# Optimization experiments

Measured on AMD Instinct MI355X. Metric: run time of the kernel, lower is better.

The kernel has to match this reference:

```python
import jax, jax.numpy as jnp
import numpy as np

N_NODES = 100000
N_EDGES = 1000000
D_IN = 64
D_OUT = 64


def setup_inputs() -> dict:
    key = jax.random.key(0)
    k_x, k_e, k_wl, k_bl, k_wr = jax.random.split(key, 5)
    x = jax.random.normal(k_x, (N_NODES, D_IN), dtype=jnp.float32)
    edge_index = jax.random.randint(k_e, (2, N_EDGES), 0, N_NODES, dtype=jnp.int64)
    scale = 1.0 / np.sqrt(D_IN)
    # SAGEConv params: lin_l (neighbor path, with bias), lin_r (root/self path, no bias)
    W_l = jax.random.uniform(k_wl, (D_OUT, D_IN), dtype=jnp.float32, minval=-scale, maxval=scale)
    b_l = jax.random.uniform(k_bl, (D_OUT,), dtype=jnp.float32, minval=-scale, maxval=scale)
    W_r = jax.random.uniform(k_wr, (D_OUT, D_IN), dtype=jnp.float32, minval=-scale, maxval=scale)
    return {"x": x, "edge_index": edge_index, "W_l": W_l, "b_l": b_l, "W_r": W_r}


def reference(x, edge_index, W_l, b_l, W_r):
    # PyG SAGEConv with mean aggregation:
    #   out = lin_l(mean_{j in N(i)} x_j) + lin_r(x_i);  then ReLU (from GCN.forward)
    src = edge_index[0]  # message sources
    dst = edge_index[1]  # aggregation targets
    n = x.shape[0]
    msg = x[src]  # [E, D_IN] gather
    agg = jax.ops.segment_sum(msg, dst, num_segments=n)  # [N, D_IN]
    deg = jax.ops.segment_sum(jnp.ones((src.shape[0],), x.dtype), dst, num_segments=n)
    mean = agg / jnp.maximum(deg, 1.0)[:, None]  # isolated nodes -> 0
    out = mean @ W_l.T + b_l + x @ W_r.T
    return jax.nn.relu(out)
```

## Files before the change

### kernel.cpp

```cpp
#include <hip/hip_runtime.h>

#define N_NODES 100000
#define N_EDGES 1000000
#define D 64

#define NFINE 782
#define CAP2 1536
#define CHUNK 4096
#define EDGE_BLOCKS 245
#define CONV_BLOCKS 6250
#define CONS_BLOCKS 1564
#define STR 132
#define SCAP 1024

typedef unsigned short u16;
typedef unsigned int u32;
using bf16x8 = __attribute__((ext_vector_type(8))) short;
using f32x4  = __attribute__((ext_vector_type(4))) float;

__device__ __forceinline__ u16 f2bf(float f) {
    u32 u = __float_as_uint(f);
    return (u16)((u + 0x7FFF + ((u >> 16) & 1)) >> 16);
}
__device__ __forceinline__ float bf2f(u16 v) {
    return __uint_as_float(((u32)v) << 16);
}

__global__ __launch_bounds__(256) void conv_zero_kernel(
    const float* __restrict__ x, u16* __restrict__ xb,
    int* __restrict__ cur2) {
    if (blockIdx.x == CONV_BLOCKS) {
        for (int j = threadIdx.x; j < NFINE; j += 256) cur2[j] = 0;
        return;
    }
    int i = blockIdx.x * 256 + threadIdx.x;
    float4 v = ((const float4*)x)[i];
    ((ushort4*)xb)[i] = make_ushort4(f2bf(v.x), f2bf(v.y), f2bf(v.z), f2bf(v.w));
}

__global__ __launch_bounds__(1024) void build3_kernel(
    const int* __restrict__ ei, int* __restrict__ cur2,
    u32* __restrict__ pairs2) {
    __shared__ u32 sorted[CHUNK];
    __shared__ u16 binof[CHUNK];
    __shared__ int hist[NFINE];
    __shared__ int off_l[NFINE];
    __shared__ int cur_l[NFINE];
    __shared__ int base_g[NFINE];
    __shared__ int wsum[16];

    int b = blockIdx.x;
    int t = threadIdx.x;
    int ln = t & 63;
    int wv = t >> 6;

    const u32* uu = (const u32*)ei;
    int f = 1;
    #pragma unroll
    for (int i = 1; i < 16; i += 2)
        if (uu[i] != 0u) f = 0;

    if (t < NFINE) hist[t] = 0;
    __syncthreads();

    int e0 = b * CHUNK;
    int e1 = min(e0 + CHUNK, N_EDGES);
    int ne = e1 - e0;

    const uint2* e64 = (const uint2*)ei;
    int srcv[4], dstv[4];
    #pragma unroll
    for (int i = 0; i < 4; i++) {
        int ee = e0 + t + i * 1024;
        bool ok = ee < e1;
        if (f) {
            uint2 sv = ok ? e64[ee] : make_uint2(0u, 0u);
            uint2 dv = ok ? e64[N_EDGES + ee] : make_uint2(0u, 0u);
            srcv[i] = (int)sv.x;
            dstv[i] = ok ? (int)dv.x : -1;
        } else {
            srcv[i] = ok ? ei[ee] : 0;
            dstv[i] = ok ? ei[N_EDGES + ee] : -1;
        }
    }
    #pragma unroll
    for (int i = 0; i < 4; i++)
        if (dstv[i] >= 0) atomicAdd(&hist[dstv[i] >> 7], 1);
    __syncthreads();

    int h = (t < NFINE) ? hist[t] : 0;
    int inc = h;
    #pragma unroll
    for (int o = 1; o < 64; o <<= 1) {
        int v = __shfl_up(inc, o);
        if (ln >= o) inc += v;
    }
    if (ln == 63) wsum[wv] = inc;
    __syncthreads();
    if (t < 16) {
        int w = wsum[t];
        int winc = w;
        #pragma unroll
        for (int o = 1; o < 16; o <<= 1) {
            int v = __shfl_up(winc, o);
            if (t >= o) winc += v;
        }
        wsum[t] = winc - w;
    }
    __syncthreads();
    if (t < NFINE) {
        int ex = inc - h + wsum[wv];
        off_l[t] = ex;
        cur_l[t] = ex;
        base_g[t] = h ? atomicAdd(&cur2[t], h) : 0;
    }
    __syncthreads();

    #pragma unroll
    for (int i = 0; i < 4; i++) {
        if (dstv[i] >= 0) {
            int fine = dstv[i] >> 7;
            int slot = atomicAdd(&cur_l[fine], 1);
            sorted[slot] = (u32)srcv[i] | ((u32)(dstv[i] & 127) << 17);
            binof[slot] = (u16)fine;
        }
    }
    __syncthreads();

    for (int i = t; i < ne; i += 1024) {
        int fine = binof[i];
        int pos = base_g[fine] + (i - off_l[fine]);
        if (pos < CAP2)
            pairs2[(size_t)fine * CAP2 + pos] = sorted[i];
    }
}

__global__ __launch_bounds__(512, 8) void cons4_kernel(
    const u16* __restrict__ xb, const float* __restrict__ Wl,
    const float* __restrict__ bl, const float* __restrict__ Wr,
    const int* __restrict__ cur2, const u32* __restrict__ pairs2,
    float* __restrict__ out) {
    __shared__ u16 Bs[64 * STR];
    __shared__ u16 As[64 * STR];
    __shared__ int sorted_s[SCAP];
    __shared__ int deg_l[64];
    __shared__ int off_l[64];
    __shared__ int cur_l[64];

    int tid = threadIdx.x;
    int bin = blockIdx.x >> 1;
    int half = blockIdx.x & 1;
    int nbase = bin * 128 + half * 64;
    if (nbase >= N_NODES) return;

    int lane = tid & 63;
    int wv = tid >> 6;

    int cnt = min(cur2[bin], CAP2);
    const u32* pb = &pairs2[(size_t)bin * CAP2];
    u32 ve[3];
    #pragma unroll
    for (int i = 0; i < 3; i++) {
        int e = tid + i * 512;
        ve[i] = (e < cnt) ? pb[e] : 0xFFFFFFFFu;
    }

    if (tid < 64) { deg_l[tid] = 0; cur_l[tid] = 0; }
    if (tid == 0) sorted_s[0] = 0;

    if (tid < 256) {
        int row = tid >> 2;
        int seg = tid & 3;
        const float4* wlf = (const float4*)Wl;
        const float4* wrf = (const float4*)Wr;
        #pragma unroll
        for (int j = 0; j < 4; j++) {
            float4 a = wlf[row * 16 + seg * 4 + j];
            float4 bq = wrf[row * 16 + seg * 4 + j];
            *(ushort4*)&Bs[row * STR + seg * 16 + j * 4] =
                make_ushort4(f2bf(a.x), f2bf(a.y), f2bf(a.z), f2bf(a.w));
            *(ushort4*)&Bs[row * STR + 64 + seg * 16 + j * 4] =
                make_ushort4(f2bf(bq.x), f2bf(bq.y), f2bf(bq.z), f2bf(bq.w));
        }
    }
    __syncthreads();

    #pragma unroll
    for (int i = 0; i < 3; i++) {
        u32 v = ve[i];
        if ((int)(v >> 23) == half) atomicAdd(&deg_l[(v >> 17) & 63], 1);
    }
    __syncthreads();

    if (tid < 64) {
        int dd = deg_l[tid];
        int inc = dd;
        #pragma unroll
        for (int o = 1; o < 64; o <<= 1) {
            int v = __shfl_up(inc, o);
            if (lane >= o) inc += v;
        }
        off_l[tid] = inc - dd;
    }
    __syncthreads();

    #pragma unroll
    for (int i = 0; i < 3; i++) {
        u32 v = ve[i];
        if ((int)(v >> 23) == half) {
            int ln = (v >> 17) & 63;
            int p = off_l[ln] + atomicAdd(&cur_l[ln], 1);
            if (p < SCAP) sorted_s[p] = (int)(v & 0x1FFFFu);
        }
    }
    __syncthreads();

    int nl8 = lane >> 3;
    int c = lane & 7;
    int nl = wv * 8 + nl8;
    int n = nbase + nl;
    int d = deg_l[nl];
    int st = off_l[nl];

    int maxd = d;
    maxd = max(maxd, __shfl_xor(maxd, 8));
    maxd = max(maxd, __shfl_xor(maxd, 16));
    maxd = max(maxd, __shfl_xor(maxd, 32));

    float acc[8];
    #pragma unroll
    for (int j = 0; j < 8; j++) acc[j] = 0.0f;

    int dm1 = (d > 0) ? (d - 1) : 0;
    int sb = (d > 0) ? st : 0;
    for (int k = 0; k < maxd; k += 4) {
        int i0 = sb + min(k + 0, dm1);
        int i1 = sb + min(k + 1, dm1);
        int i2 = sb + min(k + 2, dm1);
        int i3 = sb + min(k + 3, dm1);
        int s0 = sorted_s[i0];
        int s1 = sorted_s[i1];
        int s2 = sorted_s[i2];
        int s3 = sorted_s[i3];
        bf16x8 r0 = *(const bf16x8*)&xb[(size_t)s0 * D + c * 8];
        bf16x8 r1 = *(const bf16x8*)&xb[(size_t)s1 * D + c * 8];
        bf16x8 r2 = *(const bf16x8*)&xb[(size_t)s2 * D + c * 8];
        bf16x8 r3 = *(const bf16x8*)&xb[(size_t)s3 * D + c * 8];
        float m0 = (k + 0 < d) ? 1.0f : 0.0f;
        float m1 = (k + 1 < d) ? 1.0f : 0.0f;
        float m2 = (k + 2 < d) ? 1.0f : 0.0f;
        float m3 = (k + 3 < d) ? 1.0f : 0.0f;
        #pragma unroll
        for (int j = 0; j < 8; j++)
            acc[j] = fmaf(m0, bf2f((u16)r0[j]), acc[j]);
        #pragma unroll
        for (int j = 0; j < 8; j++)
            acc[j] = fmaf(m1, bf2f((u16)r1[j]), acc[j]);
        #pragma unroll
        for (int j = 0; j < 8; j++)
            acc[j] = fmaf(m2, bf2f((u16)r2[j]), acc[j]);
        #pragma unroll
        for (int j = 0; j < 8; j++)
            acc[j] = fmaf(m3, bf2f((u16)r3[j]), acc[j]);
    }

    float inv = (d > 0) ? (1.0f / (float)d) : 0.0f;
    bf16x8 p;
    #pragma unroll
    for (int j = 0; j < 8; j++) p[j] = (short)f2bf(acc[j] * inv);
    *(bf16x8*)&As[nl * STR + c * 8] = p;
    bf16x8 xr = {0, 0, 0, 0, 0, 0, 0, 0};
    if (n < N_NODES) xr = *(const bf16x8*)&xb[(size_t)n * D + c * 8];
    *(bf16x8*)&As[nl * STR + 64 + c * 8] = xr;
    __syncthreads();

    int mtile = wv >> 1;
    int nt0 = (wv & 1) * 2;
    int lrow = lane & 15;
    int quad = lane >> 4;

    const u16* Ab  = &As[(mtile * 16 + lrow) * STR + quad * 8];
    const u16* Bb0 = &Bs[((nt0 + 0) * 16 + lrow) * STR + quad * 8];
    const u16* Bb1 = &Bs[((nt0 + 1) * 16 + lrow) * STR + quad * 8];

    float bias0 = bl[(nt0 + 0) * 16 + lrow];
    float bias1 = bl[(nt0 + 1) * 16 + lrow];
    f32x4 acc0 = {bias0, bias0, bias0, bias0};
    f32x4 acc1 = {bias1, bias1, bias1, bias1};

    #pragma unroll
    for (int kk = 0; kk < 4; kk++) {
        bf16x8 af = *(const bf16x8*)&Ab[kk * 32];
        bf16x8 b0 = *(const bf16x8*)&Bb0[kk * 32];
        bf16x8 b1 = *(const bf16x8*)&Bb1[kk * 32];
        acc0 = __builtin_amdgcn_mfma_f32_16x16x32_bf16(af, b0, acc0, 0, 0, 0);
        acc1 = __builtin_amdgcn_mfma_f32_16x16x32_bf16(af, b1, acc1, 0, 0, 0);
    }

    int node = nbase + mtile * 16 + quad * 4;
    #pragma unroll
    for (int r = 0; r < 4; r++) {
        if (node + r < N_NODES) {
            out[(size_t)(node + r) * D + (nt0 + 0) * 16 + lrow] = fmaxf(acc0[r], 0.0f);
            out[(size_t)(node + r) * D + (nt0 + 1) * 16 + lrow] = fmaxf(acc1[r], 0.0f);
        }
    }
}

extern "C" void kernel_launch(void* const* d_in, const int* in_sizes, int n_in,
                              void* d_out, int out_size, void* d_ws, size_t ws_size,
                              hipStream_t stream) {
    const float* x  = (const float*)d_in[0];
    const int*   ei = (const int*)d_in[1];
    const float* Wl = (const float*)d_in[2];
    const float* bl = (const float*)d_in[3];
    const float* Wr = (const float*)d_in[4];
    float* out = (float*)d_out;

    char* p = (char*)d_ws;
    int* cur2   = (int*)p;                        p += 1024 * sizeof(int);
    u32* pairs2 = (u32*)p;                        p += (size_t)NFINE * CAP2 * sizeof(u32);
    u16* xb     = (u16*)p;

    conv_zero_kernel<<<CONV_BLOCKS + 1, 256, 0, stream>>>(x, xb, cur2);
    build3_kernel<<<EDGE_BLOCKS, 1024, 0, stream>>>(ei, cur2, pairs2);
    cons4_kernel<<<CONS_BLOCKS, 512, 0, stream>>>(xb, Wl, bl, Wr, cur2, pairs2, out);
}
```

Baseline: 137.6 us.

## Fuse bf16 conversion into build kernel, pad counters, degree-sort nodes, prefetch gathers

Merges the x-to-bf16 conversion blocks into the edge bucketing kernel as extra blocks and replaces the zeroing block with a hipMemsetAsync. Per-bin atomic counters are padded to 16-int stride to avoid contention on shared cache lines. The consumer kernel assigns nodes to 8-lane groups in descending-degree order so each wave's maxd loop is balanced. Its gather loop is double-buffered so the next four rows are loaded while the current four are accumulated. The costs are higher register pressure from the extra buffered rows and a 64-step rank loop per block. The conversion blocks also now run at 1024 threads, and the build blocks carry the extra shared memory.

```diff
diff --git a/kernel.cpp b/kernel.cpp
--- a/kernel.cpp
+++ b/kernel.cpp
@@ -7,14 +7,18 @@
 #define NFINE 782
 #define CAP2 1536
 #define CHUNK 4096
-#define EDGE_BLOCKS 245
-#define CONV_BLOCKS 6250
+#define BUILD_BLOCKS 245
+#define CONV_THREADS 1600000
+#define CONV_BLOCKS_F 1563
+#define FUSED_BLOCKS (BUILD_BLOCKS + CONV_BLOCKS_F)
 #define CONS_BLOCKS 1564
 #define STR 132
 #define SCAP 1024
+#define CSTR 16
 
 typedef unsigned short u16;
 typedef unsigned int u32;
+typedef unsigned char u8;
 using bf16x8 = __attribute__((ext_vector_type(8))) short;
 using f32x4  = __attribute__((ext_vector_type(4))) float;
 
@@ -26,19 +30,8 @@
     return __uint_as_float(((u32)v) << 16);
 }
 
-__global__ __launch_bounds__(256) void conv_zero_kernel(
+__global__ __launch_bounds__(1024) void conv_build_kernel(
     const float* __restrict__ x, u16* __restrict__ xb,
-    int* __restrict__ cur2) {
-    if (blockIdx.x == CONV_BLOCKS) {
-        for (int j = threadIdx.x; j < NFINE; j += 256) cur2[j] = 0;
-        return;
-    }
-    int i = blockIdx.x * 256 + threadIdx.x;
-    float4 v = ((const float4*)x)[i];
-    ((ushort4*)xb)[i] = make_ushort4(f2bf(v.x), f2bf(v.y), f2bf(v.z), f2bf(v.w));
-}
-
-__global__ __launch_bounds__(1024) void build3_kernel(
     const int* __restrict__ ei, int* __restrict__ cur2,
     u32* __restrict__ pairs2) {
     __shared__ u32 sorted[CHUNK];
@@ -48,6 +41,16 @@
     __shared__ int cur_l[NFINE];
     __shared__ int base_g[NFINE];
     __shared__ int wsum[16];
+
+    if (blockIdx.x >= BUILD_BLOCKS) {
+        int i = (blockIdx.x - BUILD_BLOCKS) * 1024 + threadIdx.x;
+        if (i < CONV_THREADS) {
+            float4 v = ((const float4*)x)[i];
+            ((ushort4*)xb)[i] =
+                make_ushort4(f2bf(v.x), f2bf(v.y), f2bf(v.z), f2bf(v.w));
+        }
+        return;
+    }
 
     int b = blockIdx.x;
     int t = threadIdx.x;
@@ -112,7 +115,7 @@
         int ex = inc - h + wsum[wv];
         off_l[t] = ex;
         cur_l[t] = ex;
-        base_g[t] = h ? atomicAdd(&cur2[t], h) : 0;
+        base_g[t] = h ? atomicAdd(&cur2[t * CSTR], h) : 0;
     }
     __syncthreads();
 
@@ -135,7 +138,7 @@
     }
 }
 
-__global__ __launch_bounds__(512, 8) void cons4_kernel(
+__global__ __launch_bounds__(512, 8) void cons5_kernel(
     const u16* __restrict__ xb, const float* __restrict__ Wl,
     const float* __restrict__ bl, const float* __restrict__ Wr,
     const int* __restrict__ cur2, const u32* __restrict__ pairs2,
@@ -146,6 +149,7 @@
     __shared__ int deg_l[64];
     __shared__ int off_l[64];
     __shared__ int cur_l[64];
+    __shared__ u8  perm_s[64];
 
     int tid = threadIdx.x;
     int bin = blockIdx.x >> 1;
@@ -156,7 +160,7 @@
     int lane = tid & 63;
     int wv = tid >> 6;
 
-    int cnt = min(cur2[bin], CAP2);
+    int cnt = min(cur2[bin * CSTR], CAP2);
     const u32* pb = &pairs2[(size_t)bin * CAP2];
     u32 ve[3];
     #pragma unroll
@@ -201,6 +205,12 @@
             if (lane >= o) inc += v;
         }
         off_l[tid] = inc - dd;
+        int rank = 0;
+        for (int j = 0; j < 64; j++) {
+            int dj = __shfl(dd, j);
+            rank += (dj > dd) || (dj == dd && j < tid);
+        }
+        perm_s[rank] = (u8)tid;
     }
     __syncthreads();
 
@@ -208,8 +218,8 @@
     for (int i = 0; i < 3; i++) {
         u32 v = ve[i];
         if ((int)(v >> 23) == half) {
-            int ln = (v >> 17) & 63;
-            int p = off_l[ln] + atomicAdd(&cur_l[ln], 1);
+            int lnn = (v >> 17) & 63;
+            int p = off_l[lnn] + atomicAdd(&cur_l[lnn], 1);
             if (p < SCAP) sorted_s[p] = (int)(v & 0x1FFFFu);
         }
     }
@@ -217,7 +227,7 @@
 
     int nl8 = lane >> 3;
     int c = lane & 7;
-    int nl = wv * 8 + nl8;
+    int nl = perm_s[wv * 8 + nl8];
     int n = nbase + nl;
     int d = deg_l[nl];
     int st = off_l[nl];
@@ -231,37 +241,70 @@
     #pragma unroll
     for (int j = 0; j < 8; j++) acc[j] = 0.0f;
 
-    int dm1 = (d > 0) ? (d - 1) : 0;
+    int dm1 = max(d - 1, 0);
     int sb = (d > 0) ? st : 0;
-    for (int k = 0; k < maxd; k += 4) {
-        int i0 = sb + min(k + 0, dm1);
-        int i1 = sb + min(k + 1, dm1);
-        int i2 = sb + min(k + 2, dm1);
-        int i3 = sb + min(k + 3, dm1);
-        int s0 = sorted_s[i0];
-        int s1 = sorted_s[i1];
-        int s2 = sorted_s[i2];
-        int s3 = sorted_s[i3];
-        bf16x8 r0 = *(const bf16x8*)&xb[(size_t)s0 * D + c * 8];
-        bf16x8 r1 = *(const bf16x8*)&xb[(size_t)s1 * D + c * 8];
-        bf16x8 r2 = *(const bf16x8*)&xb[(size_t)s2 * D + c * 8];
-        bf16x8 r3 = *(const bf16x8*)&xb[(size_t)s3 * D + c * 8];
-        float m0 = (k + 0 < d) ? 1.0f : 0.0f;
-        float m1 = (k + 1 < d) ? 1.0f : 0.0f;
-        float m2 = (k + 2 < d) ? 1.0f : 0.0f;
-        float m3 = (k + 3 < d) ? 1.0f : 0.0f;
-        #pragma unroll
-        for (int j = 0; j < 8; j++)
-            acc[j] = fmaf(m0, bf2f((u16)r0[j]), acc[j]);
-        #pragma unroll
-        for (int j = 0; j < 8; j++)
-            acc[j] = fmaf(m1, bf2f((u16)r1[j]), acc[j]);
-        #pragma unroll
-        for (int j = 0; j < 8; j++)
-            acc[j] = fmaf(m2, bf2f((u16)r2[j]), acc[j]);
-        #pragma unroll
-        for (int j = 0; j < 8; j++)
-            acc[j] = fmaf(m3, bf2f((u16)r3[j]), acc[j]);
+
+    bf16x8 rA0, rA1, rA2, rA3, rB0, rB1, rB2, rB3;
+    {
+        int s0 = sorted_s[sb + min(0, dm1)];
+        int s1 = sorted_s[sb + min(1, dm1)];
+        int s2 = sorted_s[sb + min(2, dm1)];
+        int s3 = sorted_s[sb + min(3, dm1)];
+        rA0 = *(const bf16x8*)&xb[(size_t)s0 * D + c * 8];
+        rA1 = *(const bf16x8*)&xb[(size_t)s1 * D + c * 8];
+        rA2 = *(const bf16x8*)&xb[(size_t)s2 * D + c * 8];
+        rA3 = *(const bf16x8*)&xb[(size_t)s3 * D + c * 8];
+    }
+
+    for (int k = 0; k < maxd; k += 8) {
+        {
+            int s0 = sorted_s[sb + min(k + 4, dm1)];
+            int s1 = sorted_s[sb + min(k + 5, dm1)];
+            int s2 = sorted_s[sb + min(k + 6, dm1)];
+            int s3 = sorted_s[sb + min(k + 7, dm1)];
+            rB0 = *(const bf16x8*)&xb[(size_t)s0 * D + c * 8];
+            rB1 = *(const bf16x8*)&xb[(size_t)s1 * D + c * 8];
+            rB2 = *(const bf16x8*)&xb[(size_t)s2 * D + c * 8];
+            rB3 = *(const bf16x8*)&xb[(size_t)s3 * D + c * 8];
+        }
+        {
+            float m0 = (k + 0 < d) ? 1.0f : 0.0f;
+            float m1 = (k + 1 < d) ? 1.0f : 0.0f;
+            float m2 = (k + 2 < d) ? 1.0f : 0.0f;
+            float m3 = (k + 3 < d) ? 1.0f : 0.0f;
+            #pragma unroll
+            for (int j = 0; j < 8; j++) acc[j] = fmaf(m0, bf2f((u16)rA0[j]), acc[j]);
+            #pragma unroll
+            for (int j = 0; j < 8; j++) acc[j] = fmaf(m1, bf2f((u16)rA1[j]), acc[j]);
+            #pragma unroll
+            for (int j = 0; j < 8; j++) acc[j] = fmaf(m2, bf2f((u16)rA2[j]), acc[j]);
+            #pragma unroll
+            for (int j = 0; j < 8; j++) acc[j] = fmaf(m3, bf2f((u16)rA3[j]), acc[j]);
+        }
+        if (k + 8 < maxd) {
+            int s0 = sorted_s[sb + min(k + 8,  dm1)];
+            int s1 = sorted_s[sb + min(k + 9,  dm1)];
+            int s2 = sorted_s[sb + min(k + 10, dm1)];
+            int s3 = sorted_s[sb + min(k + 11, dm1)];
+            rA0 = *(const bf16x8*)&xb[(size_t)s0 * D + c * 8];
+            rA1 = *(const bf16x8*)&xb[(size_t)s1 * D + c * 8];
+            rA2 = *(const bf16x8*)&xb[(size_t)s2 * D + c * 8];
+            rA3 = *(const bf16x8*)&xb[(size_t)s3 * D + c * 8];
+        }
+        if (k + 4 < maxd) {
+            float m0 = (k + 4 < d) ? 1.0f : 0.0f;
+            float m1 = (k + 5 < d) ? 1.0f : 0.0f;
+            float m2 = (k + 6 < d) ? 1.0f : 0.0f;
+            float m3 = (k + 7 < d) ? 1.0f : 0.0f;
+            #pragma unroll
+            for (int j = 0; j < 8; j++) acc[j] = fmaf(m0, bf2f((u16)rB0[j]), acc[j]);
+            #pragma unroll
+            for (int j = 0; j < 8; j++) acc[j] = fmaf(m1, bf2f((u16)rB1[j]), acc[j]);
+            #pragma unroll
+            for (int j = 0; j < 8; j++) acc[j] = fmaf(m2, bf2f((u16)rB2[j]), acc[j]);
+            #pragma unroll
+            for (int j = 0; j < 8; j++) acc[j] = fmaf(m3, bf2f((u16)rB3[j]), acc[j]);
+        }
     }
 
     float inv = (d > 0) ? (1.0f / (float)d) : 0.0f;
@@ -318,11 +361,11 @@
     float* out = (float*)d_out;
 
     char* p = (char*)d_ws;
-    int* cur2   = (int*)p;                        p += 1024 * sizeof(int);
+    int* cur2   = (int*)p;                        p += (size_t)NFINE * CSTR * sizeof(int);
     u32* pairs2 = (u32*)p;                        p += (size_t)NFINE * CAP2 * sizeof(u32);
     u16* xb     = (u16*)p;
 
-    conv_zero_kernel<<<CONV_BLOCKS + 1, 256, 0, stream>>>(x, xb, cur2);
-    build3_kernel<<<EDGE_BLOCKS, 1024, 0, stream>>>(ei, cur2, pairs2);
-    cons4_kernel<<<CONS_BLOCKS, 512, 0, stream>>>(xb, Wl, bl, Wr, cur2, pairs2, out);
-}
+    hipMemsetAsync(cur2, 0, (size_t)NFINE * CSTR * sizeof(int), stream);
+    conv_build_kernel<<<FUSED_BLOCKS, 1024, 0, stream>>>(x, xb, ei, cur2, pairs2);
+    cons5_kernel<<<CONS_BLOCKS, 512, 0, stream>>>(xb, Wl, bl, Wr, cur2, pairs2, out);
+}
```

Result: slower. 161.6 us (+17.4%).
